# Kernel tuning notes

Hardware: AMD Instinct MI355X
Metric: run time of the kernel (lower is better)

Reference implementation:

```python
import jax, jax.numpy as jnp
import numpy as np

B, M, DIM, HID, GRID, IMG = 32, 4096, 768, 128, 15, 240
P = GRID * GRID
NL, TOPK, BETA, EPS = 3, 10, 1.0, 1e-5


def setup_inputs() -> dict:
    key = jax.random.key(0)
    ks = jax.random.split(key, 12)
    r = lambda k, s: jax.random.normal(k, s, jnp.float32) * 0.02
    H2 = HID // 2
    return dict(
        query_tokens=jax.random.normal(ks[0], (B, P, DIM), jnp.float32),
        prompt_tokens=jax.random.normal(ks[1], (B, M, DIM), jnp.float32),
        layer_idx=0,
        sbn_g=jnp.ones((NL, DIM)), sbn_b=jnp.zeros((NL, DIM)),
        sbn_m=jnp.zeros((NL, DIM)), sbn_v=jnp.ones((NL, DIM)),
        w1=r(ks[2], (HID, DIM, 3, 3)),
        bn1_g=jnp.ones(HID), bn1_b=jnp.zeros(HID), bn1_m=jnp.zeros(HID), bn1_v=jnp.ones(HID),
        wt1=r(ks[3], (HID, HID, 2, 2)), bt1=jnp.zeros(HID),
        w2=r(ks[4], (H2, HID, 3, 3)),
        bn2_g=jnp.ones(H2), bn2_b=jnp.zeros(H2), bn2_m=jnp.zeros(H2), bn2_v=jnp.ones(H2),
        wt2=r(ks[5], (H2, H2, 2, 2)), bt2=jnp.zeros(H2),
        w3=r(ks[6], (2, H2, 1, 1)), b3=jnp.zeros(2),
        g1=r(ks[7], (HID, DIM)),
        gbn1_g=jnp.ones(HID), gbn1_b=jnp.zeros(HID), gbn1_m=jnp.zeros(HID), gbn1_v=jnp.ones(HID),
        g2=r(ks[8], (H2, HID)),
        gbn2_g=jnp.ones(H2), gbn2_b=jnp.zeros(H2), gbn2_m=jnp.zeros(H2), gbn2_v=jnp.ones(H2),
        g3=r(ks[9], (2, H2)),
    )


def _conv(x, w, pad):
    return jax.lax.conv_general_dilated(x, w, (1, 1), [(pad, pad), (pad, pad)],
                                        dimension_numbers=('NCHW', 'OIHW', 'NCHW'))


def _convT2(x, w, b):
    # ConvTranspose2d(k=2, s=2): non-overlapping -> einsum + depth-to-space
    Bn, C, H, W = x.shape
    O = w.shape[1]
    y = jnp.einsum('bchw,coij->bohiwj', x, w).reshape(Bn, O, H * 2, W * 2)
    return y + b[None, :, None, None]


def _bn2(x, g, b, m, v):
    s = g / jnp.sqrt(v + EPS)
    return (x - m[:, None, None]) * s[:, None, None] + b[:, None, None]


def _bn1(x, g, b, m, v):
    return (x - m) * (g / jnp.sqrt(v + EPS)) + b


def reference(query_tokens, prompt_tokens, layer_idx, sbn_g, sbn_b, sbn_m, sbn_v,
              w1, bn1_g, bn1_b, bn1_m, bn1_v, wt1, bt1,
              w2, bn2_g, bn2_b, bn2_m, bn2_v, wt2, bt2, w3, b3,
              g1, gbn1_g, gbn1_b, gbn1_m, gbn1_v,
              g2, gbn2_g, gbn2_b, gbn2_m, gbn2_v, g3):
    # --- align_prompt_to_query ---
    qn = query_tokens / jnp.maximum(jnp.linalg.norm(query_tokens, axis=-1, keepdims=True), 1e-12)
    pn = prompt_tokens / jnp.maximum(jnp.linalg.norm(prompt_tokens, axis=-1, keepdims=True), 1e-12)
    sim = jnp.einsum('bpd,bmd->bpm', qn, pn)            # [B,P,M]
    indices = jnp.argmax(sim, axis=-1)                  # [B,P]
    max_sim = jnp.max(sim, axis=-1)
    aligned = jnp.take_along_axis(prompt_tokens, indices[..., None], axis=1)  # [B,P,D]
    residual_map = 0.5 * (1.0 - max_sim)
    context = query_tokens + BETA * jnp.abs(query_tokens - aligned)
    # --- seg head ---
    li = min(int(layer_idx), NL - 1)
    cm = context.transpose(0, 2, 1).reshape(B, DIM, GRID, GRID)
    cm = _bn2(cm, sbn_g[li], sbn_b[li], sbn_m[li], sbn_v[li])
    h = jax.nn.relu(_bn2(_conv(cm, w1, 1), bn1_g, bn1_b, bn1_m, bn1_v))
    h = _convT2(h, wt1, bt1)                            # 15 -> 30
    h = jax.nn.relu(_bn2(_conv(h, w2, 1), bn2_g, bn2_b, bn2_m, bn2_v))
    h = _convT2(h, wt2, bt2)                            # 30 -> 60
    low = _conv(h, w3, 0) + b3[None, :, None, None]     # [B,2,60,60]
    seg = jax.image.resize(low, (B, 2, IMG, IMG), method='bilinear')  # align_corners=False
    patch_map = jax.nn.softmax(low, axis=1)[:, 1].reshape(B, -1)
    # --- global head: avg pool + topk-residual pool ---
    avg_pool = context.mean(axis=1)
    _, ti = jax.lax.top_k(residual_map, TOPK)
    topk_tokens = jnp.take_along_axis(context, ti[..., None], axis=1).mean(axis=1)
    pooled = 0.5 * avg_pool + 0.5 * topk_tokens
    g = jax.nn.relu(_bn1(pooled @ g1.T, gbn1_g, gbn1_b, gbn1_m, gbn1_v))
    g = jax.nn.relu(_bn1(g @ g2.T, gbn2_g, gbn2_b, gbn2_m, gbn2_v))
    gl = g @ g3.T
    logit = gl[:, 1] - gl[:, 0]
    return (seg, gl, logit, jax.nn.sigmoid(logit), patch_map, residual_map, context, aligned, indices)
```

## Files before the change

kernel.cpp:

```cpp
#include <hip/hip_runtime.h>
#include <cmath>

#define EPSC 1e-5f
typedef unsigned short ushortT;
typedef unsigned int uintT;
typedef __attribute__((ext_vector_type(8))) short bf16x8;
typedef __attribute__((ext_vector_type(4))) float f32x4;

constexpr size_t O_SEG   = 0;
constexpr size_t O_GL    = 3686400;
constexpr size_t O_LOGIT = 3686464;
constexpr size_t O_PROB  = 3686496;
constexpr size_t O_PATCH = 3686528;
constexpr size_t O_RES   = 3801728;
constexpr size_t O_CTX   = 3808928;
constexpr size_t O_ALN   = 9338528;
constexpr size_t O_IDX   = 14868128;

constexpr size_t WS_MS64 = 0;
constexpr size_t WS_AVG  = 14400;
constexpr size_t CB      = 38976;
constexpr size_t WS_QPK  = CB;
constexpr size_t WS_TOP2G= CB + 5898240;
constexpr size_t WS_CPH  = CB;
constexpr size_t WS_CPL  = CB + 3551232;
constexpr size_t WS_WPK  = CB + 7102464;
constexpr size_t WS_H1   = CB + 8000000;
constexpr size_t WS_T1H  = CB;
constexpr size_t WS_T1L  = CB + 2097152;
constexpr size_t WS_H2   = CB + 4200000;
constexpr size_t WS_T2   = CB + 6050000;
constexpr size_t WS_WPK2 = CB + 8950000;
constexpr size_t WS_LOW  = CB;

__global__ __launch_bounds__(256) void k_qpack(const float* __restrict__ Q,
                                               ushortT* __restrict__ qpk) {
  int id = blockIdx.x * 256 + threadIdx.x;
  int r = id & 15;
  int g = (id >> 4) & 3;
  int rest = id >> 6;
  int sub = rest % 15;
  int bkc = rest / 15;
  int kc = bkc % 24, b = bkc / 24;
  if (b >= 32) return;
  int q = sub * 16 + r;
  int k0 = kc * 32 + g * 8;
  float x[8];
  if (q < 225) {
    const float* src = Q + ((size_t)(b * 225 + q)) * 768 + k0;
#pragma unroll
    for (int e = 0; e < 8; ++e) x[e] = src[e];
  } else {
#pragma unroll
    for (int e = 0; e < 8; ++e) x[e] = 0.f;
  }
  uintT hb[8];
#pragma unroll
  for (int e = 0; e < 8; ++e) hb[e] = __float_as_uint(x[e]);
  uint4 hv;
  hv.x = (hb[0] >> 16) | (hb[1] & 0xFFFF0000u);
  hv.y = (hb[2] >> 16) | (hb[3] & 0xFFFF0000u);
  hv.z = (hb[4] >> 16) | (hb[5] & 0xFFFF0000u);
  hv.w = (hb[6] >> 16) | (hb[7] & 0xFFFF0000u);
  size_t base = ((size_t)(b * 24 + kc) * 30 + sub) * 512 + (g * 16 + r) * 8;
  *(uint4*)(qpk + base) = hv;
}

__global__ __launch_bounds__(256, 3) void k_simm(const ushortT* __restrict__ qpk,
    const float* __restrict__ PM, float4* __restrict__ top2g) {
  __shared__ ushortT sP[2 * 2048];
  __shared__ float4 smrg[240];
  __shared__ float srp[64];
  int sp = blockIdx.x, b = blockIdx.y;
  int t = threadIdx.x;
  int w = t >> 6, l = t & 63;
  int mq = t >> 3, kq = t & 7;
  const int sub0 = w * 4;
  const ushortT* qB0 = qpk + (size_t)(b * 24) * 30 * 512;

#define LOADQ(KC)                                                             \
  {                                                                           \
    const ushortT* qk = qB0 + (size_t)(KC) * (30 * 512);                      \
    _Pragma("unroll")                                                         \
    for (int ss = 0; ss < 4; ++ss) {                                          \
      int subc = sub0 + ss; if (subc > 14) subc = 14;                         \
      qh[ss] = *(const bf16x8*)(qk + subc * 512 + l * 8);                     \
    }                                                                         \
  }

#define LOADP(PR, KC)                                                         \
  {                                                                           \
    _Pragma("unroll")                                                         \
    for (int pass = 0; pass < 2; ++pass) {                                    \
      int ml = mq + pass * 32;                                                \
      PR[pass] = *(const float4*)(pmBase + (size_t)ml * 768 + (KC) * 32 + kq * 4); \
    }                                                                         \
  }

#define CVTW(PR, BUF)                                                         \
  {                                                                           \
    _Pragma("unroll")                                                         \
    for (int pass = 0; pass < 2; ++pass) {                                    \
      int ml = mq + pass * 32;                                                \
      float4 x = PR[pass];                                                    \
      pn[pass] += x.x * x.x + x.y * x.y + x.z * x.z + x.w * x.w;              \
      uintT a0 = __float_as_uint(x.x), a1 = __float_as_uint(x.y);             \
      uintT a2 = __float_as_uint(x.z), a3 = __float_as_uint(x.w);             \
      uintT h01 = (a0 >> 16) | (a1 & 0xFFFF0000u);                            \
      uintT h23 = (a2 >> 16) | (a3 & 0xFFFF0000u);                            \
      int off = (ml >> 4) * 512 + (kq >> 1) * 128 + (ml & 15) * 8 + (kq & 1) * 4; \
      *(uint2*)(&sP[(BUF) + off]) = make_uint2(h01, h23);                     \
    }                                                                         \
  }

#define MFMAPH(BUF)                                                           \
  {                                                                           \
    bf16x8 bh[4];                                                             \
    _Pragma("unroll")                                                         \
    for (int mm = 0; mm < 4; ++mm)                                            \
      bh[mm] = *(const bf16x8*)&sP[(BUF) + mm * 512 + l * 8];                 \
    _Pragma("unroll")                                                         \
    for (int ss = 0; ss < 4; ++ss) {                                          \
      if (sub0 + ss < 15) {                                                   \
        _Pragma("unroll")                                                     \
        for (int mm = 0; mm < 4; ++mm) {                                      \
          acc[ss][mm] = __builtin_amdgcn_mfma_f32_16x16x32_bf16(              \
              qh[ss], bh[mm], acc[ss][mm], 0, 0, 0);                          \
        }                                                                     \
      }                                                                       \
    }                                                                         \
  }

  f32x4 acc[4][4];
#pragma unroll
  for (int ss = 0; ss < 4; ++ss)
#pragma unroll
    for (int mm = 0; mm < 4; ++mm) acc[ss][mm] = (f32x4){0.f, 0.f, 0.f, 0.f};
  float pn[2] = {0.f, 0.f};
  const int mbase = sp * 64;
  const float* pmBase = PM + ((size_t)b * 4096 + mbase) * 768;

  bf16x8 qh[4];
  float4 pr[2];

  LOADP(pr, 0);
  CVTW(pr, 0);
  __syncthreads();

  for (int kc2 = 0; kc2 < 12; ++kc2) {
    int kc = kc2 * 2;
    LOADQ(kc);
    LOADP(pr, kc + 1);
    MFMAPH(0);
    CVTW(pr, 2048);
    __syncthreads();
    LOADQ(kc + 1);
    if (kc2 < 11) {
      LOADP(pr, kc + 2);
    }
    MFMAPH(2048);
    if (kc2 < 11) {
      CVTW(pr, 0);
    }
    __syncthreads();
  }

#pragma unroll
  for (int pass = 0; pass < 2; ++pass) {
    float v = pn[pass];
    v += __shfl_xor(v, 1); v += __shfl_xor(v, 2); v += __shfl_xor(v, 4);
    if (kq == 0) srp[mq + pass * 32] = 1.0f / fmaxf(sqrtf(v), 1e-12f);
  }
  __syncthreads();
  float rpv_[4];
#pragma unroll
  for (int mf = 0; mf < 4; ++mf) rpv_[mf] = srp[mf * 16 + (l & 15)];
#pragma unroll
  for (int ss = 0; ss < 4; ++ss) {
    int sub = sub0 + ss;
    if (sub >= 15) break;
#pragma unroll
    for (int j = 0; j < 4; ++j) {
      float a1 = -1e30f, a2 = -1e30f; int ai1 = -1, ai2 = -1;
#pragma unroll
      for (int mf = 0; mf < 4; ++mf) {
        float v = acc[ss][mf][j] * rpv_[mf];
        int mi = mbase + mf * 16 + (l & 15);
        if (v > a1) { a2 = a1; ai2 = ai1; a1 = v; ai1 = mi; }
        else if (v > a2) { a2 = v; ai2 = mi; }
      }
#pragma unroll
      for (int o = 1; o <= 8; o <<= 1) {
        float b1 = __shfl_xor(a1, o), b2 = __shfl_xor(a2, o);
        int bi1 = __shfl_xor(ai1, o), bi2 = __shfl_xor(ai2, o);
        if (b1 > a1) {
          float n2; int ni2;
          if (a1 > b2) { n2 = a1; ni2 = ai1; } else { n2 = b2; ni2 = bi2; }
          a1 = b1; ai1 = bi1; a2 = n2; ai2 = ni2;
        } else {
          if (b1 > a2) { a2 = b1; ai2 = bi1; }
        }
      }
      if ((l & 15) == j) {
        int row = sub * 16 + (l >> 4) * 4 + j;
        smrg[row] = make_float4(a1, a2, __int_as_float(ai1), __int_as_float(ai2));
      }
    }
  }
  __syncthreads();
  if (t < 240) top2g[((size_t)(b * 240 + t)) * 64 + sp] = smrg[t];
#undef LOADQ
#undef LOADP
#undef CVTW
#undef MFMAPH
}

__global__ __launch_bounds__(256) void k_refine(const float* __restrict__ Q,
    const float* __restrict__ PM, const float4* __restrict__ top2g,
    float* __restrict__ oIdx, float* __restrict__ oRes,
    float* __restrict__ oCtx, float* __restrict__ oAln,
    double* __restrict__ ms64) {
  int wid = (blockIdx.x * 256 + threadIdx.x) >> 6;
  int lane = threadIdx.x & 63;
  if (wid >= 7200) return;
  int b = wid / 225, pr = wid % 225;
  float4 e = top2g[((size_t)(b * 240 + pr)) * 64 + lane];
  float v1 = e.x, v2 = e.y;
  int i1 = __float_as_int(e.z), i2 = __float_as_int(e.w);
  int cand[8];
#pragma unroll
  for (int k = 0; k < 8; ++k) {
    float v = v1; int mi = i1;
    if (v2 > v || (v2 == v && (uintT)i2 < (uintT)mi)) { v = v2; mi = i2; }
#pragma unroll
    for (int o = 1; o <= 32; o <<= 1) {
      float ov = __shfl_xor(v, o); int omi = __shfl_xor(mi, o);
      if (ov > v || (ov == v && (uintT)omi < (uintT)mi)) { v = ov; mi = omi; }
    }
    cand[k] = mi;
    if (i1 == mi) v1 = -3e38f;
    if (i2 == mi) v2 = -3e38f;
  }
  const float* qr = Q + ((size_t)b * 225 + pr) * 768;
  float qv[12]; double nq = 0.0;
#pragma unroll
  for (int j = 0; j < 12; ++j) { float x = qr[lane + 64 * j]; qv[j] = x; nq += (double)x * (double)x; }
#pragma unroll
  for (int o = 1; o < 64; o <<= 1) nq += __shfl_xor(nq, o);
  double qn = fmax(sqrt(nq), 1e-12);
  double best = -1e300; int bi = 0;
#pragma unroll
  for (int c = 0; c < 8; ++c) {
    int mi = cand[c];
    const float* prow = PM + ((size_t)b * 4096 + mi) * 768;
    double d = 0.0, np_ = 0.0;
#pragma unroll
    for (int j = 0; j < 12; ++j) {
      double pe = (double)prow[lane + 64 * j];
      d += (double)qv[j] * pe; np_ += pe * pe;
    }
#pragma unroll
    for (int o = 1; o < 64; o <<= 1) { d += __shfl_xor(d, o); np_ += __shfl_xor(np_, o); }
    double s = d / (qn * fmax(sqrt(np_), 1e-12));
    if (s > best || (s == best && mi < bi)) { best = s; bi = mi; }
  }
  if (lane == 0) {
    oIdx[wid] = (float)bi;
    oRes[wid] = (float)(0.5 * (1.0 - best));
    ms64[wid] = best;
  }
  const float* ar = PM + ((size_t)b * 4096 + bi) * 768;
  float* cw = oCtx + (size_t)wid * 768;
  float* aw = oAln + (size_t)wid * 768;
#pragma unroll
  for (int j = 0; j < 12; ++j) {
    float a = ar[lane + 64 * j];
    float qq = qv[j];
    aw[lane + 64 * j] = a;
    cw[lane + 64 * j] = qq + fabsf(qq - a);
  }
}

__global__ __launch_bounds__(256) void k_pool(const float* __restrict__ ctx,
                                              float* __restrict__ avg) {
  int b = blockIdx.x, c = blockIdx.y, t = threadIdx.x;
  int d = c * 256 + t;
  float s = 0.f;
  for (int p = 0; p < 225; ++p) s += ctx[((size_t)b * 225 + p) * 768 + d];
  avg[b * 768 + d] = s / 225.0f;
}

__global__ __launch_bounds__(256) void k_head(const float* __restrict__ ctx,
    const double* __restrict__ ms64, const float* __restrict__ avg,
    const float* __restrict__ g1, const float* __restrict__ b1g, const float* __restrict__ b1b,
    const float* __restrict__ b1m, const float* __restrict__ b1v,
    const float* __restrict__ g2, const float* __restrict__ b2g, const float* __restrict__ b2b,
    const float* __restrict__ b2m, const float* __restrict__ b2v,
    const float* __restrict__ g3,
    float* __restrict__ oGl, float* __restrict__ oLogit, float* __restrict__ oProb) {
  __shared__ int tki[10];
  __shared__ float pooled[768];
  __shared__ float h1s[128];
  __shared__ float h2s[64];
  __shared__ float gls[2];
  int b = blockIdx.x, t = threadIdx.x;
  if (t < 64) {
    double rv[4]; int ri[4];
#pragma unroll
    for (int j = 0; j < 4; ++j) {
      int p = t + 64 * j; ri[j] = p;
      rv[j] = (p < 225) ? 0.5 * (1.0 - ms64[b * 225 + p]) : -1e300;
    }
    for (int k = 0; k < 10; ++k) {
      double bv = -1e301; int bI = 1 << 30;
#pragma unroll
      for (int j = 0; j < 4; ++j)
        if (rv[j] > bv || (rv[j] == bv && ri[j] < bI)) { bv = rv[j]; bI = ri[j]; }
#pragma unroll
      for (int o = 1; o < 64; o <<= 1) {
        double ov = __shfl_xor(bv, o); int oi = __shfl_xor(bI, o);
        if (ov > bv || (ov == bv && oi < bI)) { bv = ov; bI = oi; }
      }
      if (t == 0) tki[k] = bI;
#pragma unroll
      for (int j = 0; j < 4; ++j) if (ri[j] == bI) rv[j] = -1e300;
    }
  }
  __syncthreads();
#pragma unroll
  for (int di = 0; di < 3; ++di) {
    int d = t + di * 256;
    float s = 0.f;
    for (int k = 0; k < 10; ++k) s += ctx[((size_t)b * 225 + tki[k]) * 768 + d];
    pooled[d] = 0.5f * avg[b * 768 + d] + 0.5f * (s / 10.0f);
  }
  __syncthreads();
  if (t < 128) {
    float a = 0.f;
    for (int k = 0; k < 768; ++k) a += pooled[k] * g1[t * 768 + k];
    float sc = b1g[t] / sqrtf(b1v[t] + EPSC);
    h1s[t] = fmaxf((a - b1m[t]) * sc + b1b[t], 0.f);
  }
  __syncthreads();
  if (t < 64) {
    float a = 0.f;
    for (int k = 0; k < 128; ++k) a += h1s[k] * g2[t * 128 + k];
    float sc = b2g[t] / sqrtf(b2v[t] + EPSC);
    h2s[t] = fmaxf((a - b2m[t]) * sc + b2b[t], 0.f);
  }
  __syncthreads();
  if (t < 2) {
    float a = 0.f;
    for (int k = 0; k < 64; ++k) a += h2s[k] * g3[t * 64 + k];
    oGl[b * 2 + t] = a;
    gls[t] = a;
  }
  __syncthreads();
  if (t == 0) {
    float lg = gls[1] - gls[0];
    oLogit[b] = lg;
    oProb[b] = 1.0f / (1.0f + expf(-lg));
  }
}

__global__ __launch_bounds__(256) void k_cm2(const float* __restrict__ ctx,
    const float* __restrict__ sg, const float* __restrict__ sb,
    const float* __restrict__ sm, const float* __restrict__ sv,
    const int* __restrict__ li_p,
    ushortT* __restrict__ cph, ushortT* __restrict__ cpl) {
  int wid = (blockIdx.x * 256 + threadIdx.x) >> 6;
  int lane = threadIdx.x & 63;
  if (wid >= 7200) return;
  int b = wid / 225, s = wid % 225;
  int li = li_p[0]; li = li < 2 ? li : 2; if (li < 0) li = 0;
  int p = (s / 15 + 1) * 17 + (s % 15) + 1;
  size_t obase = ((size_t)(b * 289 + p)) * 768;
#pragma unroll
  for (int j = 0; j < 3; ++j) {
    int d0 = j * 256 + lane * 4;
    float4 x  = *(const float4*)(ctx + (size_t)wid * 768 + d0);
    float4 g4 = *(const float4*)(sg + li * 768 + d0);
    float4 v4 = *(const float4*)(sv + li * 768 + d0);
    float4 m4 = *(const float4*)(sm + li * 768 + d0);
    float4 b4 = *(const float4*)(sb + li * 768 + d0);
    float xv[4] = {x.x, x.y, x.z, x.w};
    float gv[4] = {g4.x, g4.y, g4.z, g4.w};
    float vv[4] = {v4.x, v4.y, v4.z, v4.w};
    float mv_[4] = {m4.x, m4.y, m4.z, m4.w};
    float bv_[4] = {b4.x, b4.y, b4.z, b4.w};
    ushortT hu[4], lu[4];
#pragma unroll
    for (int e = 0; e < 4; ++e) {
      float sc = gv[e] / sqrtf(vv[e] + EPSC);
      float val = (xv[e] - mv_[e]) * sc + bv_[e];
      uintT bits = __float_as_uint(val);
      float lo = val - __uint_as_float(bits & 0xFFFF0000u);
      hu[e] = (ushortT)(bits >> 16);
      lu[e] = (ushortT)(__float_as_uint(lo) >> 16);
    }
    uint2 hp, lp;
    hp.x = (uintT)hu[0] | ((uintT)hu[1] << 16);
    hp.y = (uintT)hu[2] | ((uintT)hu[3] << 16);
    lp.x = (uintT)lu[0] | ((uintT)lu[1] << 16);
    lp.y = (uintT)lu[2] | ((uintT)lu[3] << 16);
    *(uint2*)(cph + obase + d0) = hp;
    *(uint2*)(cpl + obase + d0) = lp;
  }
}

__global__ __launch_bounds__(256) void k_wpack(const float* __restrict__ w1,
                                               ushortT* __restrict__ wpk) {
  int id = blockIdx.x * 256 + threadIdx.x;
  if (id >= 110592) return;
  int ccq = id & 3;
  int o = (id >> 2) & 127;
  int pc = id >> 9;
  ushortT hu[8], lu[8];
#pragma unroll
  for (int e = 0; e < 8; ++e) {
    int c = (pc % 24) * 32 + ccq * 8 + e;
    float x = w1[((size_t)o * 768 + c) * 9 + pc / 24];
    uintT bits = __float_as_uint(x);
    float lo = x - __uint_as_float(bits & 0xFFFF0000u);
    hu[e] = (ushortT)(bits >> 16);
    lu[e] = (ushortT)(__float_as_uint(lo) >> 16);
  }
  uint4 h, lw;
  h.x = (uintT)hu[0] | ((uintT)hu[1] << 16);
  h.y = (uintT)hu[2] | ((uintT)hu[3] << 16);
  h.z = (uintT)hu[4] | ((uintT)hu[5] << 16);
  h.w = (uintT)hu[6] | ((uintT)hu[7] << 16);
  lw.x = (uintT)lu[0] | ((uintT)lu[1] << 16);
  lw.y = (uintT)lu[2] | ((uintT)lu[3] << 16);
  lw.z = (uintT)lu[4] | ((uintT)lu[5] << 16);
  lw.w = (uintT)lu[6] | ((uintT)lu[7] << 16);
  size_t base = (((size_t)pc) * 128 + o) * 32 + ccq * 8;
  *(uint4*)(wpk + base) = h;
  *(uint4*)(wpk + 884736 + base) = lw;
}

__global__ __launch_bounds__(256) void k_wpack2(const float* __restrict__ w2,
                                                ushortT* __restrict__ wpk2) {
  int id = blockIdx.x * 256 + threadIdx.x;
  if (id >= 9216) return;
  int ccq = id & 3;
  int o = (id >> 2) & 63;
  int pc = id >> 8;
  int pos = pc >> 2, ch = pc & 3;
  ushortT hu[8], lu[8];
#pragma unroll
  for (int e = 0; e < 8; ++e) {
    int c = ch * 32 + ccq * 8 + e;
    float x = w2[((size_t)o * 128 + c) * 9 + pos];
    uintT bits = __float_as_uint(x);
    float lo = x - __uint_as_float(bits & 0xFFFF0000u);
    hu[e] = (ushortT)(bits >> 16);
    lu[e] = (ushortT)(__float_as_uint(lo) >> 16);
  }
  uint4 h, lw;
  h.x = (uintT)hu[0] | ((uintT)hu[1] << 16);
  h.y = (uintT)hu[2] | ((uintT)hu[3] << 16);
  h.z = (uintT)hu[4] | ((uintT)hu[5] << 16);
  h.w = (uintT)hu[6] | ((uintT)hu[7] << 16);
  lw.x = (uintT)lu[0] | ((uintT)lu[1] << 16);
  lw.y = (uintT)lu[2] | ((uintT)lu[3] << 16);
  lw.z = (uintT)lu[4] | ((uintT)lu[5] << 16);
  lw.w = (uintT)lu[6] | ((uintT)lu[7] << 16);
  size_t base = (((size_t)pc) * 64 + o) * 32 + ccq * 8;
  *(uint4*)(wpk2 + base) = h;
  *(uint4*)(wpk2 + 73728 + base) = lw;
}

__global__ __launch_bounds__(256) void k_conv1m(
    const ushortT* __restrict__ cph, const ushortT* __restrict__ cpl,
    const ushortT* __restrict__ wpk,
    const float* __restrict__ bg, const float* __restrict__ bb,
    const float* __restrict__ bm, const float* __restrict__ bv,
    float* __restrict__ outp) {
  constexpr int ROWS = 136;
  constexpr int HSZ = ROWS * 80;
  __shared__ __align__(16) unsigned char sA[2 * HSZ];
  int band = blockIdx.x, nt = blockIdx.y, b = blockIdx.z;
  int t = threadIdx.x, w = t >> 6, l = t & 63;
  int r15 = l & 15, g = l >> 4;
  int sub = band * 4 + w;
  bool mvalid = (sub < 15);
  int p0 = ((band * 64) / 15) * 17;
  int s = sub * 16 + r15; if (s > 224) s = 224;
  int pb = (s / 15) * 17 + (s % 15) - p0;
  f32x4 acc[2];
  acc[0] = (f32x4){0.f, 0.f, 0.f, 0.f};
  acc[1] = (f32x4){0.f, 0.f, 0.f, 0.f};
  const size_t planeB = (size_t)b * 289 * 768;

  for (int ch = 0; ch < 24; ++ch) {
    __syncthreads();
    for (int i = t; i < ROWS * 8; i += 256) {
      int r = i >> 3, half = (i >> 2) & 1, seg = i & 3;
      const ushortT* src = (half ? cpl : cph) + planeB +
          (size_t)(p0 + r) * 768 + ch * 32 + seg * 8;
      uint4 v = *(const uint4*)src;
      *(uint4*)(sA + half * HSZ + r * 80 + seg * 16) = v;
    }
    __syncthreads();
#pragma unroll
    for (int pos = 0; pos < 9; ++pos) {
      const ushortT* wbh = wpk + ((size_t)(pos * 24 + ch)) * 4096;
      const ushortT* wbl = wbh + 884736;
      bf16x8 bh[2], bl[2];
#pragma unroll
      for (int nf = 0; nf < 2; ++nf) {
        int off = (nt * 32 + nf * 16 + r15) * 32 + g * 8;
        bh[nf] = *(const bf16x8*)(wbh + off);
        bl[nf] = *(const bf16x8*)(wbl + off);
      }
      int shift = (pos / 3) * 17 + (pos % 3);
      if (mvalid) {
        int row = pb + shift;
        bf16x8 ah = *(const bf16x8*)(sA + row * 80 + g * 16);
        bf16x8 al = *(const bf16x8*)(sA + HSZ + row * 80 + g * 16);
#pragma unroll
        for (int nf = 0; nf < 2; ++nf) {
          f32x4 c = acc[nf];
          c = __builtin_amdgcn_mfma_f32_16x16x32_bf16(ah, bh[nf], c, 0, 0, 0);
          c = __builtin_amdgcn_mfma_f32_16x16x32_bf16(ah, bl[nf], c, 0, 0, 0);
          c = __builtin_amdgcn_mfma_f32_16x16x32_bf16(al, bh[nf], c, 0, 0, 0);
          acc[nf] = c;
        }
      }
    }
  }
  if (mvalid) {
#pragma unroll
    for (int nf = 0; nf < 2; ++nf) {
      int o = nt * 32 + nf * 16 + r15;
      float sc = bg[o] / sqrtf(bv[o] + EPSC);
      float sh = bb[o] - bm[o] * sc;
#pragma unroll
      for (int j = 0; j < 4; ++j) {
        int srow = sub * 16 + g * 4 + j;
        if (srow < 225) {
          outp[((size_t)(b * 128 + o)) * 225 + srow] =
              fmaxf(acc[nf][j] * sc + sh, 0.f);
        }
      }
    }
  }
}

__global__ __launch_bounds__(256) void k_convT1b(const float* __restrict__ in,
    const float* __restrict__ w, const float* __restrict__ bias,
    ushortT* __restrict__ t1h, ushortT* __restrict__ t1l) {
  __shared__ float sIn[128 * 15];
  int yp = blockIdx.x, b = blockIdx.y;
  int t = threadIdx.x;
  int o = t & 127, i = t >> 7;
  for (int idx = t; idx < 128 * 15; idx += 256) {
    int c = idx / 15, x = idx % 15;
    sIn[idx] = in[((size_t)(b * 128 + c)) * 225 + yp * 15 + x];
  }
  __syncthreads();
  float acc[30];
#pragma unroll
  for (int k = 0; k < 30; ++k) acc[k] = 0.f;
  for (int c = 0; c < 128; ++c) {
    float2 wv = *(const float2*)&w[(((size_t)c * 128 + o) * 2 + i) * 2];
#pragma unroll
    for (int xx = 0; xx < 15; ++xx) {
      float iv = sIn[c * 15 + xx];
      acc[2 * xx] += wv.x * iv;
      acc[2 * xx + 1] += wv.y * iv;
    }
  }
  float bvv = bias[o];
  size_t rowb = (size_t)b * 1024 + 33 + (size_t)(2 * yp + i) * 32;
#pragma unroll
  for (int k = 0; k < 30; ++k) {
    float val = acc[k] + bvv;
    uintT bits = __float_as_uint(val);
    float lo = val - __uint_as_float(bits & 0xFFFF0000u);
    t1h[(rowb + k) * 128 + o] = (ushortT)(bits >> 16);
    t1l[(rowb + k) * 128 + o] = (ushortT)(__float_as_uint(lo) >> 16);
  }
}

__global__ __launch_bounds__(256) void k_conv2m(
    const ushortT* __restrict__ t1h, const ushortT* __restrict__ t1l,
    const ushortT* __restrict__ wpk2,
    const float* __restrict__ bg, const float* __restrict__ bb,
    const float* __restrict__ bm, const float* __restrict__ bv,
    float* __restrict__ outp) {
  constexpr int ROWS = 192;
  constexpr int HSZ = ROWS * 80;
  __shared__ __align__(16) unsigned char sA[2 * HSZ];
  int band = blockIdx.x, b = blockIdx.y;
  int t = threadIdx.x, w = t >> 6, l = t & 63;
  int r15 = l & 15, g = l >> 4;
  int sub = band * 4 + w;
  bool mvalid = (sub * 16 < 900);
  int s = sub * 16 + r15; if (s > 899) s = 899;
  int y = s / 30, x = s % 30;
  int ymin = (band * 64) / 30;
  int p0 = ymin * 32; if (p0 > 832) p0 = 832;
  int pbase = y * 32 + x - p0;
  f32x4 acc[4];
#pragma unroll
  for (int nf = 0; nf < 4; ++nf) acc[nf] = (f32x4){0.f, 0.f, 0.f, 0.f};
  const ushortT* t1hb = t1h + (size_t)b * 1024 * 128;
  const ushortT* t1lb = t1l + (size_t)b * 1024 * 128;

  for (int ch = 0; ch < 4; ++ch) {
    __syncthreads();
    for (int i = t; i < ROWS * 8; i += 256) {
      int r = i >> 3, half = (i >> 2) & 1, seg = i & 3;
      const ushortT* src = (half ? t1lb : t1hb) +
          (size_t)(p0 + r) * 128 + ch * 32 + seg * 8;
      uint4 v = *(const uint4*)src;
      *(uint4*)(sA + half * HSZ + r * 80 + seg * 16) = v;
    }
    __syncthreads();
#pragma unroll
    for (int pos = 0; pos < 9; ++pos) {
      const ushortT* wbh = wpk2 + ((size_t)(pos * 4 + ch)) * 2048;
      const ushortT* wbl = wbh + 73728;
      bf16x8 bh[4], bl[4];
#pragma unroll
      for (int nf = 0; nf < 4; ++nf) {
        int off = (nf * 16 + r15) * 32 + g * 8;
        bh[nf] = *(const bf16x8*)(wbh + off);
        bl[nf] = *(const bf16x8*)(wbl + off);
      }
      int shift = (pos / 3) * 32 + (pos % 3);
      if (mvalid) {
        int row = pbase + shift;
        bf16x8 ah = *(const bf16x8*)(sA + row * 80 + g * 16);
        bf16x8 al = *(const bf16x8*)(sA + HSZ + row * 80 + g * 16);
#pragma unroll
        for (int nf = 0; nf < 4; ++nf) {
          f32x4 c = acc[nf];
          c = __builtin_amdgcn_mfma_f32_16x16x32_bf16(ah, bh[nf], c, 0, 0, 0);
          c = __builtin_amdgcn_mfma_f32_16x16x32_bf16(ah, bl[nf], c, 0, 0, 0);
          c = __builtin_amdgcn_mfma_f32_16x16x32_bf16(al, bh[nf], c, 0, 0, 0);
          acc[nf] = c;
        }
      }
    }
  }
  if (mvalid) {
#pragma unroll
    for (int nf = 0; nf < 4; ++nf) {
      int o = nf * 16 + r15;
      float sc = bg[o] / sqrtf(bv[o] + EPSC);
      float sh = bb[o] - bm[o] * sc;
#pragma unroll
      for (int j = 0; j < 4; ++j) {
        int srow = sub * 16 + g * 4 + j;
        if (srow < 900) {
          outp[((size_t)(b * 64 + o)) * 900 + srow] =
              fmaxf(acc[nf][j] * sc + sh, 0.f);
        }
      }
    }
  }
}

template <int C, int O, int WIN, int OPLANE, int ORS, int OBASE>
__global__ __launch_bounds__(256) void k_convT(const float* __restrict__ in,
    const float* __restrict__ w, const float* __restrict__ bias, float* __restrict__ out) {
  __shared__ float sIn[C * WIN];
  int yp = blockIdx.x, b = blockIdx.y;
  int t = threadIdx.x;
  constexpr int G = 256 / O;
  constexpr int XW = WIN / (G / 2 > 0 ? G / 2 : 1);
  int o = t % O;
  int grp = t / O;
  int i = grp & 1;
  int half = grp >> 1;
  int x0 = half * XW;
  for (int idx = t; idx < C * WIN; idx += 256) {
    int c = idx / WIN, x = idx % WIN;
    sIn[idx] = in[((size_t)(b * C + c) * WIN + yp) * WIN + x];
  }
  __syncthreads();
  float acc[2 * XW];
#pragma unroll
  for (int k = 0; k < 2 * XW; ++k) acc[k] = 0.f;
  for (int c = 0; c < C; ++c) {
    float2 wv = *(const float2*)&w[(((size_t)c * O + o) * 2 + i) * 2];
#pragma unroll
    for (int xx = 0; xx < XW; ++xx) {
      float iv = sIn[c * WIN + x0 + xx];
      acc[2 * xx] += wv.x * iv;
      acc[2 * xx + 1] += wv.y * iv;
    }
  }
  float bvv = bias[o];
  float* op = out + (size_t)(b * O + o) * OPLANE + OBASE + (size_t)(2 * yp + i) * ORS + 2 * x0;
#pragma unroll
  for (int k = 0; k < 2 * XW; ++k) op[k] = acc[k] + bvv;
}

__global__ __launch_bounds__(256) void k_conv1x1(const float* __restrict__ t2,
    const float* __restrict__ w3, const float* __restrict__ b3,
    float* __restrict__ low, float* __restrict__ patch) {
  int idx = blockIdx.x * 256 + threadIdx.x;
  if (idx >= 32 * 3600) return;
  int b = idx / 3600, sp = idx % 3600;
  const float* tp = t2 + (size_t)b * 64 * 3600 + sp;
  float a0 = b3[0], a1 = b3[1];
#pragma unroll 8
  for (int c = 0; c < 64; ++c) {
    float v = tp[(size_t)c * 3600];
    a0 += v * w3[c];
    a1 += v * w3[64 + c];
  }
  low[(size_t)b * 7200 + sp] = a0;
  low[(size_t)b * 7200 + 3600 + sp] = a1;
  patch[(size_t)b * 3600 + sp] = 1.0f / (1.0f + expf(a0 - a1));
}

__global__ __launch_bounds__(256) void k_resize(const float* __restrict__ low,
                                                float* __restrict__ seg) {
  int idx = blockIdx.x * 256 + threadIdx.x;
  if (idx >= 32 * 2 * 240 * 240) return;
  int X = idx % 240;
  int Y = (idx / 240) % 240;
  int cb = idx / (240 * 240);
  const float* lp = low + (size_t)cb * 3600;
  float sy = (Y + 0.5f) * 0.25f - 0.5f;
  float sx = (X + 0.5f) * 0.25f - 0.5f;
  int y0 = (int)floorf(sy), x0 = (int)floorf(sx);
  float fy = sy - y0, fx = sx - x0;
  int y0c = min(max(y0, 0), 59), y1c = min(max(y0 + 1, 0), 59);
  int x0c = min(max(x0, 0), 59), x1c = min(max(x0 + 1, 0), 59);
  float v00 = lp[y0c * 60 + x0c], v01 = lp[y0c * 60 + x1c];
  float v10 = lp[y1c * 60 + x0c], v11 = lp[y1c * 60 + x1c];
  seg[idx] = (1.f - fy) * ((1.f - fx) * v00 + fx * v01) + fy * ((1.f - fx) * v10 + fx * v11);
}

extern "C" void kernel_launch(void* const* d_in, const int* in_sizes, int n_in,
                              void* d_out, int out_size, void* d_ws, size_t ws_size,
                              hipStream_t stream) {
  (void)in_sizes; (void)n_in; (void)out_size; (void)ws_size;
  const float* Q    = (const float*)d_in[0];
  const float* PM   = (const float*)d_in[1];
  const int*   LI   = (const int*)d_in[2];
  const float* SG   = (const float*)d_in[3];
  const float* SB   = (const float*)d_in[4];
  const float* SM   = (const float*)d_in[5];
  const float* SV   = (const float*)d_in[6];
  const float* W1   = (const float*)d_in[7];
  const float* BN1G = (const float*)d_in[8];
  const float* BN1B = (const float*)d_in[9];
  const float* BN1M = (const float*)d_in[10];
  const float* BN1V = (const float*)d_in[11];
  const float* WT1  = (const float*)d_in[12];
  const float* BT1  = (const float*)d_in[13];
  const float* W2   = (const float*)d_in[14];
  const float* BN2G = (const float*)d_in[15];
  const float* BN2B = (const float*)d_in[16];
  const float* BN2M = (const float*)d_in[17];
  const float* BN2V = (const float*)d_in[18];
  const float* WT2  = (const float*)d_in[19];
  const float* BT2  = (const float*)d_in[20];
  const float* W3   = (const float*)d_in[21];
  const float* B3   = (const float*)d_in[22];
  const float* G1   = (const float*)d_in[23];
  const float* GB1G = (const float*)d_in[24];
  const float* GB1B = (const float*)d_in[25];
  const float* GB1M = (const float*)d_in[26];
  const float* GB1V = (const float*)d_in[27];
  const float* G2   = (const float*)d_in[28];
  const float* GB2G = (const float*)d_in[29];
  const float* GB2B = (const float*)d_in[30];
  const float* GB2M = (const float*)d_in[31];
  const float* GB2V = (const float*)d_in[32];
  const float* G3   = (const float*)d_in[33];

  float* out = (float*)d_out;
  float* ws = (float*)d_ws;
  double* ms64  = (double*)(ws + WS_MS64);
  float*  avg   = ws + WS_AVG;
  ushortT* qpk  = (ushortT*)(ws + WS_QPK);
  float4* top2g = (float4*)(ws + WS_TOP2G);
  ushortT* cph  = (ushortT*)(ws + WS_CPH);
  ushortT* cpl  = (ushortT*)(ws + WS_CPL);
  ushortT* wpkp = (ushortT*)(ws + WS_WPK);
  ushortT* wpk2p= (ushortT*)(ws + WS_WPK2);
  ushortT* t1h  = (ushortT*)(ws + WS_T1H);
  ushortT* t1l  = (ushortT*)(ws + WS_T1L);
  float* h1b  = ws + WS_H1;
  float* h2b  = ws + WS_H2;
  float* t2b  = ws + WS_T2;
  float* lowb = ws + WS_LOW;

  k_qpack<<<2880, 256, 0, stream>>>(Q, qpk);
  k_simm<<<dim3(64, 32), 256, 0, stream>>>(qpk, PM, top2g);
  k_refine<<<1800, 256, 0, stream>>>(Q, PM, top2g, out + O_IDX, out + O_RES,
                                     out + O_CTX, out + O_ALN, ms64);
  k_pool<<<dim3(32, 3), 256, 0, stream>>>(out + O_CTX, avg);
  k_head<<<32, 256, 0, stream>>>(out + O_CTX, ms64, avg,
                                 G1, GB1G, GB1B, GB1M, GB1V,
                                 G2, GB2G, GB2B, GB2M, GB2V, G3,
                                 out + O_GL, out + O_LOGIT, out + O_PROB);
  k_wpack<<<432, 256, 0, stream>>>(W1, wpkp);
  k_wpack2<<<36, 256, 0, stream>>>(W2, wpk2p);
  hipMemsetAsync(ws + WS_CPH, 0, (size_t)7102464 * 4, stream);
  k_cm2<<<1800, 256, 0, stream>>>(out + O_CTX, SG, SB, SM, SV, LI, cph, cpl);
  k_conv1m<<<dim3(4, 4, 32), 256, 0, stream>>>(cph, cpl, wpkp,
                                               BN1G, BN1B, BN1M, BN1V, h1b);
  hipMemsetAsync(ws + WS_T1H, 0, (size_t)4194304 * 4, stream);
  k_convT1b<<<dim3(15, 32), 256, 0, stream>>>(h1b, WT1, BT1, t1h, t1l);
  k_conv2m<<<dim3(15, 32), 256, 0, stream>>>(t1h, t1l, wpk2p,
                                             BN2G, BN2B, BN2M, BN2V, h2b);
  k_convT<64, 64, 30, 3600, 60, 0><<<dim3(30, 32), 256, 0, stream>>>(h2b, WT2, BT2, t2b);
  k_conv1x1<<<450, 256, 0, stream>>>(t2b, W3, B3, lowb, out + O_PATCH);
  k_resize<<<14400, 256, 0, stream>>>(lowb, out + O_SEG);
}
```

Before: 593.0 us.

## Fold padding memsets into producer kernels, merge weight packs, batch refine candidates

Replaces the two full-buffer hipMemsetAsync calls with zeroing of only the padding border rows, done inside k_cm2 and k_convT1b. This avoids clearing whole padded buffers when the interiors are overwritten anyway. The two weight-pack kernels are merged into one launch. The refine kernel now handles candidates four at a time so loads and shuffle reductions can overlap. The risks are correctness if the border index maps are wrong, and higher register pressure in the refine kernel.

```diff
diff --git a/kernel.cpp b/kernel.cpp
--- a/kernel.cpp
+++ b/kernel.cpp
@@ -250,19 +250,37 @@
   double qn = fmax(sqrt(nq), 1e-12);
   double best = -1e300; int bi = 0;
 #pragma unroll
-  for (int c = 0; c < 8; ++c) {
-    int mi = cand[c];
-    const float* prow = PM + ((size_t)b * 4096 + mi) * 768;
-    double d = 0.0, np_ = 0.0;
+  for (int pass = 0; pass < 2; ++pass) {
+    const float* pp[4];
+    double d[4], nn[4];
+#pragma unroll
+    for (int c = 0; c < 4; ++c) {
+      pp[c] = PM + ((size_t)b * 4096 + cand[pass * 4 + c]) * 768 + lane;
+      d[c] = 0.0; nn[c] = 0.0;
+    }
 #pragma unroll
     for (int j = 0; j < 12; ++j) {
-      double pe = (double)prow[lane + 64 * j];
-      d += (double)qv[j] * pe; np_ += pe * pe;
-    }
-#pragma unroll
-    for (int o = 1; o < 64; o <<= 1) { d += __shfl_xor(d, o); np_ += __shfl_xor(np_, o); }
-    double s = d / (qn * fmax(sqrt(np_), 1e-12));
-    if (s > best || (s == best && mi < bi)) { best = s; bi = mi; }
+#pragma unroll
+      for (int c = 0; c < 4; ++c) {
+        double pe = (double)pp[c][64 * j];
+        d[c] += (double)qv[j] * pe;
+        nn[c] += pe * pe;
+      }
+    }
+#pragma unroll
+    for (int o = 1; o < 64; o <<= 1) {
+#pragma unroll
+      for (int c = 0; c < 4; ++c) {
+        d[c] += __shfl_xor(d[c], o);
+        nn[c] += __shfl_xor(nn[c], o);
+      }
+    }
+#pragma unroll
+    for (int c = 0; c < 4; ++c) {
+      int mi = cand[pass * 4 + c];
+      double s = d[c] / (qn * fmax(sqrt(nn[c]), 1e-12));
+      if (s > best || (s == best && mi < bi)) { best = s; bi = mi; }
+    }
   }
   if (lane == 0) {
     oIdx[wid] = (float)bi;
@@ -368,7 +386,21 @@
     const float* __restrict__ sm, const float* __restrict__ sv,
     const int* __restrict__ li_p,
     ushortT* __restrict__ cph, ushortT* __restrict__ cpl) {
-  int wid = (blockIdx.x * 256 + threadIdx.x) >> 6;
+  int id = blockIdx.x * 256 + threadIdx.x;
+  if (id < 196608) {
+    int v = id % 96;
+    int pi = (id / 96) & 63;
+    int bb = id / 6144;
+    int p = pi < 17 ? pi
+          : pi < 32 ? 17 * (pi - 16)
+          : pi < 47 ? 17 * (pi - 31) + 16
+          : 272 + (pi - 47);
+    size_t off = ((size_t)(bb * 289 + p)) * 768 + v * 8;
+    uint4 z = {0u, 0u, 0u, 0u};
+    *(uint4*)(cph + off) = z;
+    *(uint4*)(cpl + off) = z;
+  }
+  int wid = id >> 6;
   int lane = threadIdx.x & 63;
   if (wid >= 7200) return;
   int b = wid / 225, s = wid % 225;
@@ -408,67 +440,67 @@
   }
 }
 
-__global__ __launch_bounds__(256) void k_wpack(const float* __restrict__ w1,
-                                               ushortT* __restrict__ wpk) {
-  int id = blockIdx.x * 256 + threadIdx.x;
-  if (id >= 110592) return;
-  int ccq = id & 3;
-  int o = (id >> 2) & 127;
-  int pc = id >> 9;
-  ushortT hu[8], lu[8];
-#pragma unroll
-  for (int e = 0; e < 8; ++e) {
-    int c = (pc % 24) * 32 + ccq * 8 + e;
-    float x = w1[((size_t)o * 768 + c) * 9 + pc / 24];
-    uintT bits = __float_as_uint(x);
-    float lo = x - __uint_as_float(bits & 0xFFFF0000u);
-    hu[e] = (ushortT)(bits >> 16);
-    lu[e] = (ushortT)(__float_as_uint(lo) >> 16);
-  }
-  uint4 h, lw;
-  h.x = (uintT)hu[0] | ((uintT)hu[1] << 16);
-  h.y = (uintT)hu[2] | ((uintT)hu[3] << 16);
-  h.z = (uintT)hu[4] | ((uintT)hu[5] << 16);
-  h.w = (uintT)hu[6] | ((uintT)hu[7] << 16);
-  lw.x = (uintT)lu[0] | ((uintT)lu[1] << 16);
-  lw.y = (uintT)lu[2] | ((uintT)lu[3] << 16);
-  lw.z = (uintT)lu[4] | ((uintT)lu[5] << 16);
-  lw.w = (uintT)lu[6] | ((uintT)lu[7] << 16);
-  size_t base = (((size_t)pc) * 128 + o) * 32 + ccq * 8;
-  *(uint4*)(wpk + base) = h;
-  *(uint4*)(wpk + 884736 + base) = lw;
-}
-
-__global__ __launch_bounds__(256) void k_wpack2(const float* __restrict__ w2,
+__global__ __launch_bounds__(256) void k_wpackM(const float* __restrict__ w1,
+                                                const float* __restrict__ w2,
+                                                ushortT* __restrict__ wpk,
                                                 ushortT* __restrict__ wpk2) {
   int id = blockIdx.x * 256 + threadIdx.x;
-  if (id >= 9216) return;
-  int ccq = id & 3;
-  int o = (id >> 2) & 63;
-  int pc = id >> 8;
-  int pos = pc >> 2, ch = pc & 3;
-  ushortT hu[8], lu[8];
-#pragma unroll
-  for (int e = 0; e < 8; ++e) {
-    int c = ch * 32 + ccq * 8 + e;
-    float x = w2[((size_t)o * 128 + c) * 9 + pos];
-    uintT bits = __float_as_uint(x);
-    float lo = x - __uint_as_float(bits & 0xFFFF0000u);
-    hu[e] = (ushortT)(bits >> 16);
-    lu[e] = (ushortT)(__float_as_uint(lo) >> 16);
-  }
-  uint4 h, lw;
-  h.x = (uintT)hu[0] | ((uintT)hu[1] << 16);
-  h.y = (uintT)hu[2] | ((uintT)hu[3] << 16);
-  h.z = (uintT)hu[4] | ((uintT)hu[5] << 16);
-  h.w = (uintT)hu[6] | ((uintT)hu[7] << 16);
-  lw.x = (uintT)lu[0] | ((uintT)lu[1] << 16);
-  lw.y = (uintT)lu[2] | ((uintT)lu[3] << 16);
-  lw.z = (uintT)lu[4] | ((uintT)lu[5] << 16);
-  lw.w = (uintT)lu[6] | ((uintT)lu[7] << 16);
-  size_t base = (((size_t)pc) * 64 + o) * 32 + ccq * 8;
-  *(uint4*)(wpk2 + base) = h;
-  *(uint4*)(wpk2 + 73728 + base) = lw;
+  if (id < 110592) {
+    int ccq = id & 3;
+    int o = (id >> 2) & 127;
+    int pc = id >> 9;
+    ushortT hu[8], lu[8];
+#pragma unroll
+    for (int e = 0; e < 8; ++e) {
+      int c = (pc % 24) * 32 + ccq * 8 + e;
+      float x = w1[((size_t)o * 768 + c) * 9 + pc / 24];
+      uintT bits = __float_as_uint(x);
+      float lo = x - __uint_as_float(bits & 0xFFFF0000u);
+      hu[e] = (ushortT)(bits >> 16);
+      lu[e] = (ushortT)(__float_as_uint(lo) >> 16);
+    }
+    uint4 h, lw;
+    h.x = (uintT)hu[0] | ((uintT)hu[1] << 16);
+    h.y = (uintT)hu[2] | ((uintT)hu[3] << 16);
+    h.z = (uintT)hu[4] | ((uintT)hu[5] << 16);
+    h.w = (uintT)hu[6] | ((uintT)hu[7] << 16);
+    lw.x = (uintT)lu[0] | ((uintT)lu[1] << 16);
+    lw.y = (uintT)lu[2] | ((uintT)lu[3] << 16);
+    lw.z = (uintT)lu[4] | ((uintT)lu[5] << 16);
+    lw.w = (uintT)lu[6] | ((uintT)lu[7] << 16);
+    size_t base = (((size_t)pc) * 128 + o) * 32 + ccq * 8;
+    *(uint4*)(wpk + base) = h;
+    *(uint4*)(wpk + 884736 + base) = lw;
+  } else {
+    int id2 = id - 110592;
+    if (id2 >= 9216) return;
+    int ccq = id2 & 3;
+    int o = (id2 >> 2) & 63;
+    int pc = id2 >> 8;
+    int pos = pc >> 2, ch = pc & 3;
+    ushortT hu[8], lu[8];
+#pragma unroll
+    for (int e = 0; e < 8; ++e) {
+      int c = ch * 32 + ccq * 8 + e;
+      float x = w2[((size_t)o * 128 + c) * 9 + pos];
+      uintT bits = __float_as_uint(x);
+      float lo = x - __uint_as_float(bits & 0xFFFF0000u);
+      hu[e] = (ushortT)(bits >> 16);
+      lu[e] = (ushortT)(__float_as_uint(lo) >> 16);
+    }
+    uint4 h, lw;
+    h.x = (uintT)hu[0] | ((uintT)hu[1] << 16);
+    h.y = (uintT)hu[2] | ((uintT)hu[3] << 16);
+    h.z = (uintT)hu[4] | ((uintT)hu[5] << 16);
+    h.w = (uintT)hu[6] | ((uintT)hu[7] << 16);
+    lw.x = (uintT)lu[0] | ((uintT)lu[1] << 16);
+    lw.y = (uintT)lu[2] | ((uintT)lu[3] << 16);
+    lw.z = (uintT)lu[4] | ((uintT)lu[5] << 16);
+    lw.w = (uintT)lu[6] | ((uintT)lu[7] << 16);
+    size_t base = (((size_t)pc) * 64 + o) * 32 + ccq * 8;
+    *(uint4*)(wpk2 + base) = h;
+    *(uint4*)(wpk2 + 73728 + base) = lw;
+  }
 }
 
 __global__ __launch_bounds__(256) void k_conv1m(
@@ -554,6 +586,22 @@
   __shared__ float sIn[128 * 15];
   int yp = blockIdx.x, b = blockIdx.y;
   int t = threadIdx.x;
+  {
+    int flat = (b * 15 + yp) * 256 + t;
+    if (flat < 63488) {
+      int v = flat & 15;
+      int pi = (flat >> 4) % 124;
+      int bb = flat / 1984;
+      int p = pi < 32 ? pi
+            : pi < 62 ? 32 * (pi - 31)
+            : pi < 92 ? 32 * (pi - 61) + 31
+            : 992 + (pi - 92);
+      size_t off = ((size_t)bb * 1024 + p) * 128 + v * 8;
+      uint4 z = {0u, 0u, 0u, 0u};
+      *(uint4*)(t1h + off) = z;
+      *(uint4*)(t1l + off) = z;
+    }
+  }
   int o = t & 127, i = t >> 7;
   for (int idx = t; idx < 128 * 15; idx += 256) {
     int c = idx / 15, x = idx % 15;
@@ -803,13 +851,10 @@
                                  G1, GB1G, GB1B, GB1M, GB1V,
                                  G2, GB2G, GB2B, GB2M, GB2V, G3,
                                  out + O_GL, out + O_LOGIT, out + O_PROB);
-  k_wpack<<<432, 256, 0, stream>>>(W1, wpkp);
-  k_wpack2<<<36, 256, 0, stream>>>(W2, wpk2p);
-  hipMemsetAsync(ws + WS_CPH, 0, (size_t)7102464 * 4, stream);
+  k_wpackM<<<468, 256, 0, stream>>>(W1, W2, wpkp, wpk2p);
   k_cm2<<<1800, 256, 0, stream>>>(out + O_CTX, SG, SB, SM, SV, LI, cph, cpl);
   k_conv1m<<<dim3(4, 4, 32), 256, 0, stream>>>(cph, cpl, wpkp,
                                                BN1G, BN1B, BN1M, BN1V, h1b);
-  hipMemsetAsync(ws + WS_T1H, 0, (size_t)4194304 * 4, stream);
   k_convT1b<<<dim3(15, 32), 256, 0, stream>>>(h1b, WT1, BT1, t1h, t1l);
   k_conv2m<<<dim3(15, 32), 256, 0, stream>>>(t1h, t1l, wpk2p,
                                              BN2G, BN2B, BN2M, BN2V, h2b);
```

Result: faster. 570.2 us (-3.8%).
